# Optimization experiments

Measured on AMD Instinct MI355X. Metric: run time of the kernel, lower is better.

Reference implementation:

```python
import jax, jax.numpy as jnp
import numpy as np

P_CONST = 10.0   # opt.p
SCALE = 0.1      # opt.output_scale
WD = 0.0005      # opt.weight_decay


def _proj(M, X):
    # orthogonal projection onto tangent space of Stiefel manifold at M
    A = M.T @ X
    A_sym = 0.5 * (A + A.T)
    return X - M @ A_sym


def _lstm_cell(x, h0, c0, Wih, Whh, bih, bhh):
    # single-timestep LSTM cell, PyTorch gate order (i, f, g, o)
    g = x @ Wih.T + h0 @ Whh.T + bih + bhh  # (k, 4H)
    i, f, gg, o = jnp.split(g, 4, axis=-1)
    c = jax.nn.sigmoid(f) * c0 + jax.nn.sigmoid(i) * jnp.tanh(gg)
    h = jax.nn.sigmoid(o) * jnp.tanh(c)
    return h, c


def setup_inputs() -> dict:
    key = jax.random.key(0)
    ks = jax.random.split(key, 16)
    H = 20
    k_dim = 3 * 3 * 512  # 4608 = prod of trailing dims of s

    def rn(k, shape, s=1.0):
        return jax.random.normal(k, shape, dtype=jnp.float32) * s

    return {
        "e": rn(ks[0], (4096, 4096)),
        "e_grad": rn(ks[1], (4096, 4096), 0.01),
        "s": rn(ks[2], (512, 3, 3, 512)),
        "s_grad": rn(ks[3], (512, 3, 3, 512), 0.01),
        "L_h0": rn(ks[4], (2, k_dim, H)),
        "L_c0": rn(ks[5], (2, k_dim, H)),
        "L_before": rn(ks[6], (k_dim, k_dim), 0.1),
        "W_ih0": rn(ks[7], (4 * H, 1), 0.2),
        "W_hh0": rn(ks[8], (4 * H, H), 0.2),
        "b_ih0": rn(ks[9], (4 * H,), 0.1),
        "b_hh0": rn(ks[10], (4 * H,), 0.1),
        "W_ih1": rn(ks[11], (4 * H, H), 0.2),
        "W_hh1": rn(ks[12], (4 * H, H), 0.2),
        "b_ih1": rn(ks[13], (4 * H,), 0.1),
        "b_hh1": rn(ks[14], (4 * H,), 0.1),
        "Wl": rn(ks[15], (1, H), 0.2),
        "bl": jnp.zeros((1,), jnp.float32),
        "e_lr": jnp.float32(0.01),
        "s_lr": jnp.float32(0.01),
    }


def reference(e, e_grad, s, s_grad, L_h0, L_c0, L_before,
              W_ih0, W_hh0, b_ih0, b_hh0, W_ih1, W_hh1, b_ih1, b_hh1,
              Wl, bl, e_lr, s_lr):
    # --- euclidean params: SGD with weight decay ---
    new_e = e - e_lr * (e_grad + WD * e)

    # --- Stiefel param update ---
    n0 = s.shape[0]
    M = s.reshape(n0, -1).T                 # (k, n0)
    Mg = -s_lr * s_grad.reshape(n0, -1).T   # (k, n0)
    G = _proj(M, Mg)                        # (k, n0)

    # LogAndSign preprocessing: only the diagonal of G G^T is consumed
    diag_ggt = jnp.einsum('ij,ij->i', G, G)                      # diag(G @ G.T), (k,)
    x = jnp.clip(jnp.log(jnp.abs(diag_ggt)) / P_CONST, -1.0, 1.0)[:, None]  # (k,1)

    # 2-layer LSTM, one timestep, batch = k
    h0n, c0n = _lstm_cell(x, L_h0[0], L_c0[0], W_ih0, W_hh0, b_ih0, b_hh0)
    h1n, c1n = _lstm_cell(h0n, L_h0[1], L_c0[1], W_ih1, W_hh1, b_ih1, b_hh1)

    l = (h1n @ Wl.T + bl) * SCALE           # (k,1)
    l = (l - l.mean() + 1.0)[:, 0]          # (k,)
    L = jnp.maximum(jnp.diag(l), L_before)  # (k,k)

    P = _proj(M, L @ G)                     # (k, n0)

    # QR retraction with sign fix
    Q, R = jnp.linalg.qr(M + P)             # reduced: Q (k, n0), R (n0, n0)
    sgn = jnp.sign(jnp.sign(jnp.diagonal(R)) + 0.5)
    new_s = (Q * sgn[None, :]).T.reshape(s.shape)

    hn = jnp.stack([h0n, h1n])
    cn = jnp.stack([c0n, c1n])
    return new_e, new_s, L, hn, cn
```

## Files before the change

kernel.cpp:

```cpp
#include <hip/hip_runtime.h>
#include <math.h>

#define KD 4608
#define N0 512
#define WDECAY 0.0005f

#define OFF_E  0
#define OFF_S  16777216
#define OFF_L  19136512
#define OFF_HN 40370176
#define OFF_CN 40554496

__device__ __forceinline__ float sigf(float x){ return 1.0f/(1.0f+expf(-x)); }

__global__ __launch_bounds__(256) void new_e_kernel(
    float* __restrict__ out, const float* __restrict__ e,
    const float* __restrict__ g, const float* __restrict__ lrp)
{
  const float lr = lrp[0];
  const float a = 1.0f - lr * WDECAY;
  size_t i = ((size_t)blockIdx.x * 256 + threadIdx.x) * 4;
  float4 ev = *(const float4*)(e + i);
  float4 gv = *(const float4*)(g + i);
  float4 o;
  o.x = ev.x * a - lr * gv.x;
  o.y = ev.y * a - lr * gv.y;
  o.z = ev.z * a - lr * gv.z;
  o.w = ev.w * a - lr * gv.w;
  *(float4*)(out + i) = o;
}

__global__ __launch_bounds__(256) void transpose_k(
    float* __restrict__ dst, const float* __restrict__ src,
    int R, int Cc, const float* scale_ptr, float scale_const)
{
  __shared__ float tile[32][33];
  float s = scale_const * (scale_ptr ? scale_ptr[0] : 1.0f);
  int c0 = blockIdx.x * 32, r0 = blockIdx.y * 32;
  int tx = threadIdx.x, ty = threadIdx.y;
#pragma unroll
  for (int i = 0; i < 32; i += 8)
    tile[ty + i][tx] = src[(size_t)(r0 + ty + i) * Cc + c0 + tx] * s;
  __syncthreads();
#pragma unroll
  for (int i = 0; i < 32; i += 8)
    dst[(size_t)(c0 + ty + i) * R + r0 + tx] = tile[tx][ty + i];
}

__global__ __launch_bounds__(256) void gemm_tn_splitk(
    float* __restrict__ out, const float* __restrict__ X,
    const float* __restrict__ Y, int Kchunk)
{
  __shared__ float Xs[16][64];
  __shared__ float Ys[16][64];
  const int tid = threadIdx.x;
  const int tx = tid & 15, ty = tid >> 4;
  const int a0 = blockIdx.x * 64, b0 = blockIdx.y * 64;
  const int k0 = blockIdx.z * Kchunk;
  const int lk = tid >> 4, lc = (tid & 15) << 2;
  float acc[4][4] = {};
  for (int kk = 0; kk < Kchunk; kk += 16){
    *(float4*)&Xs[lk][lc] = *(const float4*)&X[(size_t)(k0+kk+lk)*512 + a0 + lc];
    *(float4*)&Ys[lk][lc] = *(const float4*)&Y[(size_t)(k0+kk+lk)*512 + b0 + lc];
    __syncthreads();
#pragma unroll
    for (int k = 0; k < 16; ++k){
      float4 a4 = *(const float4*)&Xs[k][ty<<2];
      float4 b4 = *(const float4*)&Ys[k][tx<<2];
      float av[4] = {a4.x,a4.y,a4.z,a4.w};
      float bv[4] = {b4.x,b4.y,b4.z,b4.w};
#pragma unroll
      for (int i=0;i<4;i++)
#pragma unroll
        for (int j=0;j<4;j++)
          acc[i][j] += av[i]*bv[j];
    }
    __syncthreads();
  }
#pragma unroll
  for (int i=0;i<4;i++)
#pragma unroll
    for (int j=0;j<4;j++)
      atomicAdd(&out[(size_t)(a0+(ty<<2)+i)*512 + b0+(tx<<2)+j], acc[i][j]);
}

__global__ __launch_bounds__(256) void sym_kernel(
    float* __restrict__ out, const float* __restrict__ A)
{
  int idx = blockIdx.x * 256 + threadIdx.x;
  int a = idx >> 9, b = idx & 511;
  out[idx] = 0.5f * (A[idx] + A[b*512 + a]);
}

template<int TN>
__global__ __launch_bounds__(256) void gemm_nn(
    float* __restrict__ D, const float* __restrict__ A,
    const float* __restrict__ Bm, const float* __restrict__ C0,
    float alpha, float beta, int K, int lda)
{
  constexpr int WN = TN/16;
  __shared__ float As[16][64];
  __shared__ float Bs[16][TN];
  const int tid = threadIdx.x;
  const int tx = tid & 15, ty = tid >> 4;
  const int m0 = blockIdx.x * 64, n0 = blockIdx.y * TN;
  const int ar = tid >> 2, ak = (tid & 3) << 2;
  constexpr int BPR = TN/4;
  const int bk = tid / BPR;
  const int bn = (tid % BPR) << 2;
  constexpr int BP = (16*BPR)/256;
  constexpr int BKSTEP = 256/BPR;
  float acc[4][WN];
#pragma unroll
  for (int i=0;i<4;i++)
#pragma unroll
    for (int j=0;j<WN;j++) acc[i][j]=0.f;

  for (int k0 = 0; k0 < K; k0 += 16){
    float4 av = *(const float4*)&A[(size_t)(m0+ar)*lda + k0 + ak];
    As[ak+0][ar]=av.x; As[ak+1][ar]=av.y; As[ak+2][ar]=av.z; As[ak+3][ar]=av.w;
#pragma unroll
    for (int p=0;p<BP;p++){
      int kk = bk + p*BKSTEP;
      *(float4*)&Bs[kk][bn] = *(const float4*)&Bm[(size_t)(k0+kk)*512 + n0 + bn];
    }
    __syncthreads();
#pragma unroll
    for (int k=0;k<16;k++){
      float4 a4 = *(const float4*)&As[k][ty<<2];
      float av2[4] = {a4.x,a4.y,a4.z,a4.w};
      float bv[WN];
#pragma unroll
      for (int j=0;j<WN;j+=4){
        float4 b4 = *(const float4*)&Bs[k][tx*WN + j];
        bv[j]=b4.x; bv[j+1]=b4.y; bv[j+2]=b4.z; bv[j+3]=b4.w;
      }
#pragma unroll
      for (int i=0;i<4;i++)
#pragma unroll
        for (int j=0;j<WN;j++)
          acc[i][j] += av2[i]*bv[j];
    }
    __syncthreads();
  }
#pragma unroll
  for (int i=0;i<4;i++){
    int r = m0 + (ty<<2) + i;
#pragma unroll
    for (int j=0;j<WN;j++){
      int c = n0 + tx*WN + j;
      float v = alpha * acc[i][j];
      if (C0) v += beta * C0[(size_t)r*512 + c];
      D[(size_t)r*512 + c] = v;
    }
  }
}

__global__ __launch_bounds__(256) void rowsq_kernel(
    const float* __restrict__ G, float* __restrict__ x)
{
  int row = blockIdx.x * 4 + (threadIdx.x >> 6);
  int lane = threadIdx.x & 63;
  const float* g = G + (size_t)row * 512;
  float s = 0.f;
#pragma unroll
  for (int t = 0; t < 8; ++t){ float v = g[lane + t*64]; s += v*v; }
  for (int off = 32; off; off >>= 1) s += __shfl_down(s, off, 64);
  if (lane == 0){
    float v = logf(fabsf(s)) * 0.1f;
    x[row] = fminf(fmaxf(v, -1.f), 1.f);
  }
}

__global__ __launch_bounds__(256) void lstm_kernel(
    const float* __restrict__ x, const float* __restrict__ Lh,
    const float* __restrict__ Lc,
    const float* __restrict__ Wih0, const float* __restrict__ Whh0,
    const float* __restrict__ bih0, const float* __restrict__ bhh0,
    const float* __restrict__ Wih1, const float* __restrict__ Whh1,
    const float* __restrict__ bih1, const float* __restrict__ bhh1,
    const float* __restrict__ Wl, const float* __restrict__ bl,
    float* __restrict__ out_hn, float* __restrict__ out_cn,
    float* __restrict__ lp)
{
  __shared__ float sWih0[80], sWhh0[1600], sb0[80];
  __shared__ float sWih1[1600], sWhh1[1600], sb1[80];
  __shared__ float sWl[20], sbl;
  int tid = threadIdx.x;
  for (int t = tid; t < 80; t += 256){
    sWih0[t] = Wih0[t];
    sb0[t] = bih0[t] + bhh0[t];
    sb1[t] = bih1[t] + bhh1[t];
  }
  for (int t = tid; t < 1600; t += 256){
    sWhh0[t] = Whh0[t];
    sWih1[t] = Wih1[t];
    sWhh1[t] = Whh1[t];
  }
  if (tid < 20) sWl[tid] = Wl[tid];
  if (tid == 0) sbl = bl[0];
  __syncthreads();
  int b = blockIdx.x * 256 + tid;
  const float xv = x[b];
  float hp[20], h0n[20];
#pragma unroll
  for (int c = 0; c < 20; ++c) hp[c] = Lh[b*20 + c];
#pragma unroll
  for (int c = 0; c < 20; ++c){
    float gi = xv * sWih0[c]      + sb0[c];
    float gf = xv * sWih0[20 + c] + sb0[20 + c];
    float gg = xv * sWih0[40 + c] + sb0[40 + c];
    float go = xv * sWih0[60 + c] + sb0[60 + c];
#pragma unroll
    for (int k = 0; k < 20; ++k){
      float h = hp[k];
      gi += h * sWhh0[c*20 + k];
      gf += h * sWhh0[(20 + c)*20 + k];
      gg += h * sWhh0[(40 + c)*20 + k];
      go += h * sWhh0[(60 + c)*20 + k];
    }
    float c0v = Lc[b*20 + c];
    float cn = sigf(gf) * c0v + sigf(gi) * tanhf(gg);
    float hn = sigf(go) * tanhf(cn);
    out_hn[b*20 + c] = hn;
    out_cn[b*20 + c] = cn;
    h0n[c] = hn;
  }
  float hp1[20];
#pragma unroll
  for (int c = 0; c < 20; ++c) hp1[c] = Lh[92160 + b*20 + c];
  float lacc = sbl;
#pragma unroll
  for (int c = 0; c < 20; ++c){
    float gi = sb1[c], gf = sb1[20+c], gg = sb1[40+c], go = sb1[60+c];
#pragma unroll
    for (int k = 0; k < 20; ++k){
      float a0 = h0n[k], a1 = hp1[k];
      gi += a0 * sWih1[c*20 + k]      + a1 * sWhh1[c*20 + k];
      gf += a0 * sWih1[(20+c)*20 + k] + a1 * sWhh1[(20+c)*20 + k];
      gg += a0 * sWih1[(40+c)*20 + k] + a1 * sWhh1[(40+c)*20 + k];
      go += a0 * sWih1[(60+c)*20 + k] + a1 * sWhh1[(60+c)*20 + k];
    }
    float c0v = Lc[92160 + b*20 + c];
    float cn = sigf(gf) * c0v + sigf(gi) * tanhf(gg);
    float hn = sigf(go) * tanhf(cn);
    out_hn[92160 + b*20 + c] = hn;
    out_cn[92160 + b*20 + c] = cn;
    lacc += hn * sWl[c];
  }
  lp[b] = lacc * 0.1f;
}

__global__ __launch_bounds__(256) void mean_kernel(
    const float* __restrict__ lp, float* __restrict__ meanout)
{
  __shared__ float red[4];
  int tid = threadIdx.x;
  float s = 0.f;
  for (int i = tid; i < KD; i += 256) s += lp[i];
  for (int off = 32; off; off >>= 1) s += __shfl_down(s, off, 64);
  if ((tid & 63) == 0) red[tid >> 6] = s;
  __syncthreads();
  if (tid == 0) meanout[0] = (red[0]+red[1]+red[2]+red[3]) * (1.0f/4608.0f);
}

__global__ __launch_bounds__(256) void build_L_kernel(
    float* __restrict__ outL, const float* __restrict__ Lb,
    const float* __restrict__ lp, const float* __restrict__ meanp)
{
  size_t idx = (size_t)blockIdx.x * 256 + threadIdx.x;
  int i = (int)(idx / 1152);
  int j = (int)(idx % 1152) * 4;
  float li = lp[i] - meanp[0] + 1.0f;
  float4 lb = *(const float4*)&Lb[(size_t)i*KD + j];
  float4 o;
  o.x = fmaxf(lb.x, (j+0 == i) ? li : 0.f);
  o.y = fmaxf(lb.y, (j+1 == i) ? li : 0.f);
  o.z = fmaxf(lb.z, (j+2 == i) ? li : 0.f);
  o.w = fmaxf(lb.w, (j+3 == i) ? li : 0.f);
  *(float4*)&outL[(size_t)i*KD + j] = o;
}

__global__ __launch_bounds__(256) void add_kernel(
    float* __restrict__ B, const float* __restrict__ M)
{
  size_t i = ((size_t)blockIdx.x * 256 + threadIdx.x) * 4;
  float4 b = *(const float4*)(B + i);
  float4 m = *(const float4*)(M + i);
  b.x += m.x; b.y += m.y; b.z += m.z; b.w += m.w;
  *(float4*)(B + i) = b;
}

__global__ __launch_bounds__(256) void chol_factor(
    float* __restrict__ C, float* __restrict__ invLg, int kb)
{
  __shared__ float T[64][65];
  __shared__ float W[64][65];
  const int tid = threadIdx.x;
  const int base = kb * 64;
  for (int t = tid; t < 4096; t += 256)
    T[t>>6][t&63] = C[(size_t)(base + (t>>6))*512 + base + (t&63)];
  __syncthreads();
  const int i = tid & 63, q = tid >> 6;
  for (int j = 0; j < 64; ++j){
    float dj = sqrtf(T[j][j]);
    __syncthreads();
    if (q == 0){
      if (i == j) T[j][j] = dj;
      else if (i > j) T[i][j] /= dj;
    }
    __syncthreads();
    if (i > j){
      float lij = T[i][j];
      for (int jj = j+1+q; jj <= i; jj += 4)
        T[i][jj] -= lij * T[jj][j];
    }
    __syncthreads();
  }
  if (q == 0){
    const int j = i;
    for (int r = 0; r < j; ++r) W[r][j] = 0.f;
    W[j][j] = 1.0f / T[j][j];
    for (int r = j+1; r < 64; ++r){
      float ssum = 0.f;
      for (int k = j; k < r; ++k) ssum += T[r][k] * W[k][j];
      W[r][j] = -ssum / T[r][r];
    }
  }
  __syncthreads();
  for (int t = tid; t < 4096; t += 256){
    int r = t >> 6, c = t & 63;
    C[(size_t)(base + r)*512 + base + c] = T[r][c];
    invLg[kb*4096 + t] = W[r][c];
  }
}

__global__ __launch_bounds__(256) void chol_trsm(
    float* __restrict__ C, const float* __restrict__ invLg, int kb)
{
  __shared__ float Ts[64][65];
  __shared__ float Ws[64][65];
  const int tid = threadIdx.x;
  const int r0 = 64*(kb+1) + blockIdx.x * 64;
  const int cb = kb * 64;
  for (int t = tid; t < 1024; t += 256){
    int r = t >> 4, qd = (t & 15) << 2;
    float4 v = *(const float4*)&C[(size_t)(r0+r)*512 + cb + qd];
    Ts[r][qd]=v.x; Ts[r][qd+1]=v.y; Ts[r][qd+2]=v.z; Ts[r][qd+3]=v.w;
    float4 w = *(const float4*)&invLg[kb*4096 + r*64 + qd];
    Ws[r][qd]=w.x; Ws[r][qd+1]=w.y; Ws[r][qd+2]=w.z; Ws[r][qd+3]=w.w;
  }
  __syncthreads();
  const int tx = tid & 15, ty = tid >> 4;
  float acc[4][4] = {};
#pragma unroll 8
  for (int k = 0; k < 64; ++k){
    float a_[4], b_[4];
#pragma unroll
    for (int i=0;i<4;i++){ a_[i] = Ts[(ty<<2)+i][k]; b_[i] = Ws[(tx<<2)+i][k]; }
#pragma unroll
    for (int i=0;i<4;i++)
#pragma unroll
      for (int j=0;j<4;j++)
        acc[i][j] += a_[i]*b_[j];
  }
#pragma unroll
  for (int i=0;i<4;i++)
#pragma unroll
    for (int j=0;j<4;j++)
      C[(size_t)(r0+(ty<<2)+i)*512 + cb + (tx<<2)+j] = acc[i][j];
}

__global__ __launch_bounds__(256) void chol_syrk(float* __restrict__ C, int kb)
{
  if (blockIdx.y > blockIdx.x) return;
  __shared__ float Ar[64][65];
  __shared__ float Ac[64][65];
  const int tid = threadIdx.x;
  const int base = 64*(kb+1);
  const int r0 = base + blockIdx.x * 64, c0 = base + blockIdx.y * 64;
  const int cb = kb * 64;
  for (int t = tid; t < 1024; t += 256){
    int r = t >> 4, qd = (t & 15) << 2;
    float4 v = *(const float4*)&C[(size_t)(r0+r)*512 + cb + qd];
    Ar[r][qd]=v.x; Ar[r][qd+1]=v.y; Ar[r][qd+2]=v.z; Ar[r][qd+3]=v.w;
    float4 w = *(const float4*)&C[(size_t)(c0+r)*512 + cb + qd];
    Ac[r][qd]=w.x; Ac[r][qd+1]=w.y; Ac[r][qd+2]=w.z; Ac[r][qd+3]=w.w;
  }
  __syncthreads();
  const int tx = tid & 15, ty = tid >> 4;
  float acc[4][4] = {};
#pragma unroll 8
  for (int k = 0; k < 64; ++k){
    float a_[4], b_[4];
#pragma unroll
    for (int i=0;i<4;i++){ a_[i] = Ar[(ty<<2)+i][k]; b_[i] = Ac[(tx<<2)+i][k]; }
#pragma unroll
    for (int i=0;i<4;i++)
#pragma unroll
      for (int j=0;j<4;j++)
        acc[i][j] += a_[i]*b_[j];
  }
#pragma unroll
  for (int i=0;i<4;i++)
#pragma unroll
    for (int j=0;j<4;j++){
      size_t o = (size_t)(r0+(ty<<2)+i)*512 + c0 + (tx<<2)+j;
      C[o] -= acc[i][j];
    }
}

__global__ __launch_bounds__(256) void panel_q(
    float* __restrict__ Q, const float* __restrict__ B,
    const float* __restrict__ Lc, const float* __restrict__ invLg, int jb)
{
  __shared__ float Qs[16][64];
  __shared__ float Rs[16][68];
  __shared__ float Ts[64][65];
  __shared__ float Ws[64][65];
  const int tid = threadIdx.x;
  const int tx = tid & 15, ty = tid >> 4;
  const int r0 = blockIdx.x * 64;
  const int cb = jb * 64;
  for (int t = tid; t < 4096; t += 256)
    Ws[t>>6][t&63] = invLg[jb*4096 + t];
  float acc[4][4] = {};
  const int lr = tid >> 2, lk = (tid & 3) << 2;
  for (int k0 = 0; k0 < cb; k0 += 16){
    float4 qv = *(const float4*)&Q[(size_t)(r0+lr)*512 + k0 + lk];
    Qs[lk+0][lr]=qv.x; Qs[lk+1][lr]=qv.y; Qs[lk+2][lr]=qv.z; Qs[lk+3][lr]=qv.w;
    float4 rv = *(const float4*)&Lc[(size_t)(cb+lr)*512 + k0 + lk];
    Rs[lk+0][lr]=rv.x; Rs[lk+1][lr]=rv.y; Rs[lk+2][lr]=rv.z; Rs[lk+3][lr]=rv.w;
    __syncthreads();
#pragma unroll
    for (int k = 0; k < 16; ++k){
      float4 a4 = *(const float4*)&Qs[k][ty<<2];
      float av[4] = {a4.x,a4.y,a4.z,a4.w};
      float bv[4];
#pragma unroll
      for (int j=0;j<4;j++) bv[j] = Rs[k][(tx<<2)+j];
#pragma unroll
      for (int i=0;i<4;i++)
#pragma unroll
        for (int j=0;j<4;j++)
          acc[i][j] += av[i]*bv[j];
    }
    __syncthreads();
  }
#pragma unroll
  for (int i=0;i<4;i++){
    int r = (ty<<2)+i;
#pragma unroll
    for (int j=0;j<4;j++){
      int c = (tx<<2)+j;
      Ts[r][c] = B[(size_t)(r0+r)*512 + cb + c] - acc[i][j];
    }
  }
  __syncthreads();
  float acc2[4][4] = {};
#pragma unroll 8
  for (int k = 0; k < 64; ++k){
    float a_[4], b_[4];
#pragma unroll
    for (int i=0;i<4;i++){ a_[i] = Ts[(ty<<2)+i][k]; b_[i] = Ws[(tx<<2)+i][k]; }
#pragma unroll
    for (int i=0;i<4;i++)
#pragma unroll
      for (int j=0;j<4;j++)
        acc2[i][j] += a_[i]*b_[j];
  }
#pragma unroll
  for (int i=0;i<4;i++)
#pragma unroll
    for (int j=0;j<4;j++)
      Q[(size_t)(r0+(ty<<2)+i)*512 + cb + (tx<<2)+j] = acc2[i][j];
}

extern "C" void kernel_launch(void* const* d_in, const int* in_sizes, int n_in,
                              void* d_out, int out_size, void* d_ws, size_t ws_size,
                              hipStream_t stream) {
  const float* e      = (const float*)d_in[0];
  const float* e_grad = (const float*)d_in[1];
  const float* s      = (const float*)d_in[2];
  const float* s_grad = (const float*)d_in[3];
  const float* L_h0   = (const float*)d_in[4];
  const float* L_c0   = (const float*)d_in[5];
  const float* L_before = (const float*)d_in[6];
  const float* W_ih0  = (const float*)d_in[7];
  const float* W_hh0  = (const float*)d_in[8];
  const float* b_ih0  = (const float*)d_in[9];
  const float* b_hh0  = (const float*)d_in[10];
  const float* W_ih1  = (const float*)d_in[11];
  const float* W_hh1  = (const float*)d_in[12];
  const float* b_ih1  = (const float*)d_in[13];
  const float* b_hh1  = (const float*)d_in[14];
  const float* Wl     = (const float*)d_in[15];
  const float* bl     = (const float*)d_in[16];
  const float* e_lr   = (const float*)d_in[17];
  const float* s_lr   = (const float*)d_in[18];

  float* out = (float*)d_out;
  float* out_e  = out + OFF_E;
  float* out_s  = out + OFF_S;
  float* out_L  = out + OFF_L;
  float* out_hn = out + OFF_HN;
  float* out_cn = out + OFF_CN;

  float* ws   = (float*)d_ws;
  float* M    = ws;
  float* Bb   = ws + 2359296;
  float* G    = ws + 4718592;
  float* Abuf = ws + 7077888;
  float* Asym = ws + 7340032;
  float* Cb   = ws + 7602176;
  float* invL = ws + 7864320;
  float* xb   = ws + 7897088;
  float* lp   = ws + 7901696;
  float* meanb= ws + 7906304;

  new_e_kernel<<<16384, 256, 0, stream>>>(out_e, e, e_grad, e_lr);
  transpose_k<<<dim3(144,16), dim3(32,8), 0, stream>>>(M, s, 512, KD, nullptr, 1.0f);
  transpose_k<<<dim3(144,16), dim3(32,8), 0, stream>>>(Bb, s_grad, 512, KD, s_lr, -1.0f);
  hipMemsetAsync(Abuf, 0, 262144*sizeof(float), stream);
  gemm_tn_splitk<<<dim3(8,8,9), 256, 0, stream>>>(Abuf, M, Bb, 512);
  sym_kernel<<<1024, 256, 0, stream>>>(Asym, Abuf);
  gemm_nn<64><<<dim3(72,8), 256, 0, stream>>>(G, M, Asym, Bb, -1.f, 1.f, 512, 512);
  rowsq_kernel<<<1152, 256, 0, stream>>>(G, xb);
  lstm_kernel<<<18, 256, 0, stream>>>(xb, L_h0, L_c0, W_ih0, W_hh0, b_ih0, b_hh0,
                                      W_ih1, W_hh1, b_ih1, b_hh1, Wl, bl,
                                      out_hn, out_cn, lp);
  mean_kernel<<<1, 256, 0, stream>>>(lp, meanb);
  build_L_kernel<<<20736, 256, 0, stream>>>(out_L, L_before, lp, meanb);
  gemm_nn<128><<<dim3(72,4), 256, 0, stream>>>(Bb, out_L, G, nullptr, 1.f, 0.f, KD, KD);
  hipMemsetAsync(Abuf, 0, 262144*sizeof(float), stream);
  gemm_tn_splitk<<<dim3(8,8,9), 256, 0, stream>>>(Abuf, M, Bb, 512);
  sym_kernel<<<1024, 256, 0, stream>>>(Asym, Abuf);
  add_kernel<<<2304, 256, 0, stream>>>(Bb, M);
  gemm_nn<64><<<dim3(72,8), 256, 0, stream>>>(Bb, M, Asym, Bb, -1.f, 1.f, 512, 512);
  hipMemsetAsync(Cb, 0, 262144*sizeof(float), stream);
  gemm_tn_splitk<<<dim3(8,8,9), 256, 0, stream>>>(Cb, Bb, Bb, 512);
  for (int kb = 0; kb < 8; ++kb){
    chol_factor<<<1, 256, 0, stream>>>(Cb, invL, kb);
    int rem = 7 - kb;
    if (rem > 0){
      chol_trsm<<<rem, 256, 0, stream>>>(Cb, invL, kb);
      chol_syrk<<<dim3(rem, rem), 256, 0, stream>>>(Cb, kb);
    }
  }
  for (int jb = 0; jb < 8; ++jb)
    panel_q<<<72, 256, 0, stream>>>(G, Bb, Cb, invL, jb);
  transpose_k<<<dim3(16,144), dim3(32,8), 0, stream>>>(out_s, G, KD, 512, nullptr, 1.0f);
}
```

Baseline: 2.114 ms.

## Compute L@G with bf16 MFMA using bf16 copies of L and transposed G

Adds a bf16 MFMA GEMM for the large L(4608x4608) @ G product. build_L now also writes a bf16 copy of L, and a new transpose kernel writes a bf16 copy of G transposed. Operands are loaded straight into LDS with global_load_lds. The aim is to replace the fp32 FMA GEMM, which dominates runtime, with matrix cores and halve operand bandwidth. The cost is bf16 rounding feeding the QR retraction, which may break tolerance, plus an extra bf16 write of L. The path is gated on workspace size.

```diff
diff --git a/kernel.cpp b/kernel.cpp
--- a/kernel.cpp
+++ b/kernel.cpp
@@ -11,7 +11,23 @@
 #define OFF_HN 40370176
 #define OFF_CN 40554496
 
+typedef unsigned short ushort_t;
+typedef __attribute__((ext_vector_type(8))) short bf16x8;
+typedef __attribute__((ext_vector_type(4))) float f32x4;
+
 __device__ __forceinline__ float sigf(float x){ return 1.0f/(1.0f+expf(-x)); }
+
+__device__ __forceinline__ unsigned short cvt_bf16(float x){
+  unsigned int u = __float_as_uint(x);
+  unsigned int r = (u + 0x7FFFu + ((u >> 16) & 1u)) >> 16;
+  return (unsigned short)r;
+}
+
+__device__ __forceinline__ void gload_lds16(const void* g, void* l){
+  __builtin_amdgcn_global_load_lds(
+      (const __attribute__((address_space(1))) unsigned int*)g,
+      (__attribute__((address_space(3))) unsigned int*)l, 16, 0, 0);
+}
 
 __global__ __launch_bounds__(256) void new_e_kernel(
     float* __restrict__ out, const float* __restrict__ e,
@@ -45,6 +61,21 @@
 #pragma unroll
   for (int i = 0; i < 32; i += 8)
     dst[(size_t)(c0 + ty + i) * R + r0 + tx] = tile[tx][ty + i];
+}
+
+__global__ __launch_bounds__(256) void transpose_cvt_bf16(
+    ushort_t* __restrict__ dst, const float* __restrict__ src, int R, int Cc)
+{
+  __shared__ float tile[32][33];
+  int c0 = blockIdx.x * 32, r0 = blockIdx.y * 32;
+  int tx = threadIdx.x, ty = threadIdx.y;
+#pragma unroll
+  for (int i = 0; i < 32; i += 8)
+    tile[ty + i][tx] = src[(size_t)(r0 + ty + i) * Cc + c0 + tx];
+  __syncthreads();
+#pragma unroll
+  for (int i = 0; i < 32; i += 8)
+    dst[(size_t)(c0 + ty + i) * R + r0 + tx] = cvt_bf16(tile[tx][ty + i]);
 }
 
 __global__ __launch_bounds__(256) void gemm_tn_splitk(
@@ -156,6 +187,44 @@
   }
 }
 
+__global__ __launch_bounds__(256) void gemm_LG_mfma(
+    float* __restrict__ C, const ushort_t* __restrict__ Lb,
+    const ushort_t* __restrict__ Gt)
+{
+  __shared__ ushort_t As[64*32];
+  __shared__ ushort_t Bs[64*32];
+  const int id = blockIdx.x;
+  const int mb = (id & 7) + 8 * (id >> 6);
+  const int nb = (id >> 3) & 7;
+  const int tid = threadIdx.x;
+  const int w = tid >> 6, lane = tid & 63;
+  const int m0 = mb * 64, n0 = nb * 64;
+  f32x4 acc[4] = {};
+  const ushort_t* gA = Lb + (size_t)(m0 + (tid >> 2)) * KD + (tid & 3) * 8;
+  const ushort_t* gB = Gt + (size_t)(n0 + (tid >> 2)) * KD + (tid & 3) * 8;
+  ushort_t* lA = As + tid * 8;
+  ushort_t* lB = Bs + tid * 8;
+  const int mrow = lane & 15, kq = lane >> 4;
+  const int aoff = mrow * 32 + kq * 8;
+  for (int k0 = 0; k0 < KD; k0 += 32){
+    gload_lds16(gA + k0, lA);
+    gload_lds16(gB + k0, lB);
+    __syncthreads();
+    bf16x8 bfrag = *(const bf16x8*)&Bs[w * 16 * 32 + aoff];
+#pragma unroll
+    for (int mt = 0; mt < 4; ++mt){
+      bf16x8 afrag = *(const bf16x8*)&As[mt * 16 * 32 + aoff];
+      acc[mt] = __builtin_amdgcn_mfma_f32_16x16x32_bf16(afrag, bfrag, acc[mt], 0, 0, 0);
+    }
+    __syncthreads();
+  }
+#pragma unroll
+  for (int mt = 0; mt < 4; ++mt)
+#pragma unroll
+    for (int r = 0; r < 4; ++r)
+      C[(size_t)(m0 + mt*16 + kq*4 + r) * 512 + n0 + w*16 + mrow] = acc[mt][r];
+}
+
 __global__ __launch_bounds__(256) void rowsq_kernel(
     const float* __restrict__ G, float* __restrict__ x)
 {
@@ -265,7 +334,8 @@
 }
 
 __global__ __launch_bounds__(256) void build_L_kernel(
-    float* __restrict__ outL, const float* __restrict__ Lb,
+    float* __restrict__ outL, ushort_t* __restrict__ outLbf,
+    const float* __restrict__ Lb,
     const float* __restrict__ lp, const float* __restrict__ meanp)
 {
   size_t idx = (size_t)blockIdx.x * 256 + threadIdx.x;
@@ -279,6 +349,12 @@
   o.z = fmaxf(lb.z, (j+2 == i) ? li : 0.f);
   o.w = fmaxf(lb.w, (j+3 == i) ? li : 0.f);
   *(float4*)&outL[(size_t)i*KD + j] = o;
+  if (outLbf){
+    ushort_t b0 = cvt_bf16(o.x), b1 = cvt_bf16(o.y), b2 = cvt_bf16(o.z), b3 = cvt_bf16(o.w);
+    unsigned int p0 = (unsigned int)b0 | ((unsigned int)b1 << 16);
+    unsigned int p1 = (unsigned int)b2 | ((unsigned int)b3 << 16);
+    *(uint2*)&outLbf[(size_t)i*KD + j] = make_uint2(p0, p1);
+  }
 }
 
 __global__ __launch_bounds__(256) void add_kernel(
@@ -517,6 +593,9 @@
   float* xb   = ws + 7897088;
   float* lp   = ws + 7901696;
   float* meanb= ws + 7906304;
+  ushort_t* Lbf = (ushort_t*)(ws + 7906560);
+  ushort_t* Gt  = (ushort_t*)(ws + 7906560 + 10616832);
+  const bool use_mfma = ws_size >= (size_t)(7906560 + 10616832 + 1179648) * 4;
 
   new_e_kernel<<<16384, 256, 0, stream>>>(out_e, e, e_grad, e_lr);
   transpose_k<<<dim3(144,16), dim3(32,8), 0, stream>>>(M, s, 512, KD, nullptr, 1.0f);
@@ -526,12 +605,18 @@
   sym_kernel<<<1024, 256, 0, stream>>>(Asym, Abuf);
   gemm_nn<64><<<dim3(72,8), 256, 0, stream>>>(G, M, Asym, Bb, -1.f, 1.f, 512, 512);
   rowsq_kernel<<<1152, 256, 0, stream>>>(G, xb);
+  if (use_mfma)
+    transpose_cvt_bf16<<<dim3(16,144), dim3(32,8), 0, stream>>>(Gt, G, KD, 512);
   lstm_kernel<<<18, 256, 0, stream>>>(xb, L_h0, L_c0, W_ih0, W_hh0, b_ih0, b_hh0,
                                       W_ih1, W_hh1, b_ih1, b_hh1, Wl, bl,
                                       out_hn, out_cn, lp);
   mean_kernel<<<1, 256, 0, stream>>>(lp, meanb);
-  build_L_kernel<<<20736, 256, 0, stream>>>(out_L, L_before, lp, meanb);
-  gemm_nn<128><<<dim3(72,4), 256, 0, stream>>>(Bb, out_L, G, nullptr, 1.f, 0.f, KD, KD);
+  build_L_kernel<<<20736, 256, 0, stream>>>(out_L, use_mfma ? Lbf : nullptr,
+                                            L_before, lp, meanb);
+  if (use_mfma)
+    gemm_LG_mfma<<<576, 256, 0, stream>>>(Bb, Lbf, Gt);
+  else
+    gemm_nn<128><<<dim3(72,4), 256, 0, stream>>>(Bb, out_L, G, nullptr, 1.f, 0.f, KD, KD);
   hipMemsetAsync(Abuf, 0, 262144*sizeof(float), stream);
   gemm_tn_splitk<<<dim3(8,8,9), 256, 0, stream>>>(Abuf, M, Bb, 512);
   sym_kernel<<<1024, 256, 0, stream>>>(Asym, Abuf);
```

Result: faster. 1.720 ms (-18.6%).
